# Kernel tuning notes

Hardware: AMD Instinct MI355X
Metric: run time of the kernel (lower is better)

## Reference

```python
import math
import jax, jax.numpy as jnp
import numpy as np

D_MODEL = 1024
D_K = 64
D_V = 64
N_HEADS = 16
D_HIDDEN = 4096
EPS = 1e-5


def setup_inputs() -> dict:
    key = jax.random.key(0)
    ks = jax.random.split(key, 10)
    s = 0.02
    x = jax.random.normal(ks[0], (2, 2048, D_MODEL), dtype=jnp.float32)
    wq = jax.random.normal(ks[1], (D_MODEL, D_K * N_HEADS), jnp.float32) * s
    bq = jnp.zeros((D_K * N_HEADS,), jnp.float32)
    wk = jax.random.normal(ks[2], (D_MODEL, D_K * N_HEADS), jnp.float32) * s
    bk = jnp.zeros((D_K * N_HEADS,), jnp.float32)
    wv = jax.random.normal(ks[3], (D_MODEL, D_V * N_HEADS), jnp.float32) * s
    bv = jnp.zeros((D_V * N_HEADS,), jnp.float32)
    wo = jax.random.normal(ks[4], (D_V * N_HEADS, D_MODEL), jnp.float32) * s
    ln1_g = jnp.ones((D_MODEL,), jnp.float32)
    ln1_b = jnp.zeros((D_MODEL,), jnp.float32)
    w1 = jax.random.normal(ks[5], (D_MODEL, D_HIDDEN), jnp.float32) * s
    b1 = jnp.zeros((D_HIDDEN,), jnp.float32)
    w2 = jax.random.normal(ks[6], (D_HIDDEN, D_MODEL), jnp.float32) * s
    ln2_g = jnp.ones((D_MODEL,), jnp.float32)
    ln2_b = jnp.zeros((D_MODEL,), jnp.float32)
    return dict(x=x, wq=wq, bq=bq, wk=wk, bk=bk, wv=wv, bv=bv, wo=wo,
                ln1_g=ln1_g, ln1_b=ln1_b, w1=w1, b1=b1, w2=w2,
                ln2_g=ln2_g, ln2_b=ln2_b)


def _layernorm(x, g, b):
    mu = jnp.mean(x, axis=-1, keepdims=True)
    var = jnp.mean((x - mu) ** 2, axis=-1, keepdims=True)
    return (x - mu) * jax.lax.rsqrt(var + EPS) * g + b


def reference(x, wq, bq, wk, bk, wv, bv, wo, ln1_g, ln1_b, w1, b1, w2, ln2_g, ln2_b):
    B, S, _ = x.shape
    split = lambda t, d: t.reshape(B, S, N_HEADS, d).transpose(0, 2, 1, 3)  # [B,H,S,d]
    Q = split(x @ wq + bq, D_K)
    K = split(x @ wk + bk, D_K)
    V = split(x @ wv + bv, D_V)
    scores = jnp.einsum('bhqd,bhkd->bhqk', Q / math.sqrt(D_K), K)
    causal = jnp.tril(jnp.ones((S, S), dtype=bool))
    scores = jnp.where(causal, scores, -jnp.inf)
    attn = jax.nn.softmax(scores, axis=-1)
    ctx = jnp.einsum('bhqk,bhkd->bhqd', attn, V)  # [B,H,S,d_v]
    merged = ctx.transpose(0, 2, 1, 3).reshape(B, S, N_HEADS * D_V)
    x = x + _layernorm(merged @ wo, ln1_g, ln1_b)
    h = jax.nn.gelu(x @ w1 + b1, approximate=False)
    x = x + _layernorm(h @ w2, ln2_g, ln2_b)
    return x
```

## Files before the change

### kernel.cpp

```cpp
#include <hip/hip_runtime.h>
#include <math.h>

typedef __bf16 bf16;
typedef __bf16 bf16x4 __attribute__((ext_vector_type(4)));
typedef __bf16 bf16x8 __attribute__((ext_vector_type(8)));
typedef float f32x4 __attribute__((ext_vector_type(4)));

#define MFMA16(a, b, c) __builtin_amdgcn_mfma_f32_16x16x32_bf16(a, b, c, 0, 0, 0)
#define QSCALE 0.180336879f
#define SSTR 3072
#define SOFT_M -14.0f

typedef __attribute__((address_space(3))) unsigned int lds_uint;
typedef const __attribute__((address_space(1))) unsigned int glb_uint;
__device__ __forceinline__ void gload_lds16(const void* g, void* l) {
    __builtin_amdgcn_global_load_lds((glb_uint*)g, (lds_uint*)l, 16, 0, 0);
}
__device__ __forceinline__ unsigned lds_addr(const void* p) {
    return (unsigned)(unsigned long long)(lds_uint*)p;
}

__global__ __launch_bounds__(256) void prep_kernel(
    const float* __restrict__ x,
    const float* __restrict__ wq, const float* __restrict__ wk,
    const float* __restrict__ wv, const float* __restrict__ wo,
    const float* __restrict__ w1, const float* __restrict__ w2,
    const float* __restrict__ bq, const float* __restrict__ bk,
    const float* __restrict__ bv,
    bf16* __restrict__ xbf, bf16* __restrict__ wqkvt, bf16* __restrict__ wot,
    bf16* __restrict__ w1t, bf16* __restrict__ w2t, float* __restrict__ bqkv) {
    const int bid = blockIdx.x, tid = threadIdx.x;
    if (bid < 4096) {
        size_t i = ((size_t)bid * 256 + tid) * 4;
        float4 v = *(const float4*)(x + i);
        bf16x4 o = {(bf16)v.x, (bf16)v.y, (bf16)v.z, (bf16)v.w};
        *(bf16x4*)(xbf + i) = o;
        return;
    }
    if (bid < 16384) {
        __shared__ float tile[32][33];
        const float* W; bf16* Wt; int K, N, n0, k0;
        if (bid < 8192) {
            int l = bid - 4096, z = l >> 10, t = l & 1023;
            W = z == 0 ? wq : z == 1 ? wk : z == 2 ? wv : wo;
            Wt = z == 3 ? wot : wqkvt + (size_t)z * 1024 * 1024;
            K = 1024; N = 1024; n0 = (t & 31) * 32; k0 = (t >> 5) * 32;
        } else if (bid < 12288) {
            int l = bid - 8192;
            W = w1; Wt = w1t; K = 1024; N = 4096;
            n0 = (l & 127) * 32; k0 = (l >> 7) * 32;
        } else {
            int l = bid - 12288;
            W = w2; Wt = w2t; K = 4096; N = 1024;
            n0 = (l & 31) * 32; k0 = (l >> 5) * 32;
        }
        const int tx = tid & 31, ty = tid >> 5;
        for (int i = 0; i < 32; i += 8)
            tile[ty + i][tx] = W[(size_t)(k0 + ty + i) * N + n0 + tx];
        __syncthreads();
        for (int i = 0; i < 32; i += 8)
            Wt[(size_t)(n0 + ty + i) * K + k0 + tx] = (bf16)tile[tx][ty + i];
        return;
    }
    int i = (bid - 16384) * 256 + tid;
    bqkv[i] = i < 1024 ? bq[i] : i < 2048 ? bk[i - 1024] : bv[i - 2048];
}

__global__ void transpose_v_kernel(const bf16* __restrict__ QKV, bf16* __restrict__ Vtg) {
    __shared__ bf16 t[64 * 64];
    const int tid = threadIdx.x;
    const int st = blockIdx.x;
    const int bh = blockIdx.y;
    const int b = bh >> 4, h = bh & 15;
    const bf16* src = QKV + (size_t)b * 2048 * SSTR + 2048 + h * 64 + (size_t)st * 64 * SSTR;
    const int s = tid >> 3, oct = tid & 7;
    bf16x8 v0 = *(const bf16x8*)&src[(size_t)s * SSTR + oct * 8];
    bf16x8 v1 = *(const bf16x8*)&src[(size_t)(s + 32) * SSTR + oct * 8];
    *(bf16x8*)&t[s * 64 + ((oct ^ (s & 7)) * 8)] = v0;
    *(bf16x8*)&t[(s + 32) * 64 + ((oct ^ (s & 7)) * 8)] = v1;
    __syncthreads();
    const int dv = tid >> 3, so = tid & 7;
    bf16 b0[8], b1[8];
#pragma unroll
    for (int j = 0; j < 8; j++) {
        int ss = (so & 4) * 8 + (so & 3) * 4 + (j < 4 ? j : 12 + j);
        b0[j] = t[ss * 64 + (((dv >> 3) ^ (ss & 7)) * 8) + (dv & 7)];
        b1[j] = t[ss * 64 + ((((dv + 32) >> 3) ^ (ss & 7)) * 8) + (dv & 7)];
    }
    bf16* dst = Vtg + (size_t)bh * 64 * 2048 + (size_t)st * 64;
    *(bf16x8*)&dst[(size_t)dv * 2048 + so * 8] = *(bf16x8*)b0;
    *(bf16x8*)&dst[(size_t)(dv + 32) * 2048 + so * 8] = *(bf16x8*)b1;
}

template <bool HAS_BIAS, bool DO_GELU, bool OUT_BF16, bool QKV_SCALE, int NSPLIT>
__global__ __launch_bounds__(256, 4) void gemm_nt(
    const bf16* __restrict__ A, const bf16* __restrict__ Bt,
    const float* __restrict__ bias,
    float* __restrict__ Cf, bf16* __restrict__ Cb,
    int M, int N, int K) {
    __shared__ bf16 As[2][128 * 32];
    __shared__ bf16 Bs[2][128 * 32];
    const int tid = threadIdx.x;
    const int wave = tid >> 6, lane = tid & 63;
    const int ln = lane & 15, quad = lane >> 4;
    const int GN = N >> 7;
    const int nblk = gridDim.x;
    const int bid = blockIdx.x;
    const int lid = (bid & 7) * (nblk >> 3) + (bid >> 3);
    const int ngroup = GN * 8;
    const int g = lid / ngroup, rem = lid - g * ngroup;
    const int m0 = (g * 8 + (rem & 7)) * 128;
    const int n0 = (rem >> 3) * 128;
    const int wm = (wave >> 1) * 64, wn = (wave & 1) * 64;
    int kz0 = 0, kz1 = K;
    if (NSPLIT > 1) {
        const int kchunk = K / NSPLIT;
        kz0 = blockIdx.z * kchunk;
        kz1 = kz0 + kchunk;
        if (OUT_BF16) Cb += (size_t)blockIdx.z * M * N;
        else          Cf += (size_t)blockIdx.z * M * N;
    }
    const int srow0 = wave * 32 + (lane >> 2);
    const int srow1 = srow0 + 16;
    const int soct = ((lane & 3) ^ (srow0 & 3)) * 8;
    const bf16* ga0 = A + (size_t)(m0 + srow0) * K + soct;
    const bf16* ga1 = A + (size_t)(m0 + srow1) * K + soct;
    const bf16* gb0 = Bt + (size_t)(n0 + srow0) * K + soct;
    const bf16* gb1 = Bt + (size_t)(n0 + srow1) * K + soct;

    f32x4 acc[4][4] = {};
    const int roct = (quad ^ (ln & 3)) * 8;

#define GSTAGE(k0_, bi_)                                        \
    {                                                           \
        bf16* la = As[bi_] + wave * 1024;                       \
        bf16* lb = Bs[bi_] + wave * 1024;                       \
        gload_lds16(ga0 + (k0_), la);                           \
        gload_lds16(ga1 + (k0_), la + 512);                     \
        gload_lds16(gb0 + (k0_), lb);                           \
        gload_lds16(gb1 + (k0_), lb + 512);                     \
    }

    GSTAGE(kz0, 0)
    int it = 0;
    for (int k0 = kz0; k0 < kz1; k0 += 32, ++it) {
        const int cur = it & 1;
        __syncthreads();
        if (k0 + 32 < kz1) GSTAGE(k0 + 32, cur ^ 1)
        bf16x8 af[4], bg[4];
#pragma unroll
        for (int i = 0; i < 4; i++) {
            af[i] = *(const bf16x8*)&As[cur][(wm + i * 16 + ln) * 32 + roct];
            bg[i] = *(const bf16x8*)&Bs[cur][(wn + i * 16 + ln) * 32 + roct];
        }
#pragma unroll
        for (int i = 0; i < 4; i++)
#pragma unroll
            for (int j = 0; j < 4; j++)
                acc[i][j] = MFMA16(af[i], bg[j], acc[i][j]);
    }
#undef GSTAGE

#pragma unroll
    for (int i = 0; i < 4; i++)
#pragma unroll
        for (int j = 0; j < 4; j++) {
            int col = n0 + wn + j * 16 + ln;
            float bv = HAS_BIAS ? bias[col] : 0.0f;
#pragma unroll
            for (int r = 0; r < 4; r++) {
                int row = m0 + wm + i * 16 + quad * 4 + r;
                float v = acc[i][j][r] + bv;
                if (QKV_SCALE && col < 1024) v *= QSCALE;
                if (DO_GELU) {
                    float u = v * (v * v * 0.044715f + 1.0f) * 0.7978845608f;
                    float t = __builtin_amdgcn_exp2f(u * 2.885390082f);
                    v = v * t * __builtin_amdgcn_rcpf(t + 1.0f);
                }
                if (OUT_BF16)
                    Cb[(size_t)row * N + col] = (bf16)v;
                else
                    Cf[(size_t)row * N + col] = v;
            }
        }
}

#define BARR() __builtin_amdgcn_s_barrier()
#define WAITLG(n_) { asm volatile("s_waitcnt lgkmcnt(" #n_ ")" ::: "memory"); \
                     __builtin_amdgcn_sched_barrier(0); }
#define WAITVM(n_) asm volatile("s_waitcnt vmcnt(" #n_ ")" ::: "memory")
#define PRIO1() __builtin_amdgcn_s_setprio(1)
#define PRIO0() __builtin_amdgcn_s_setprio(0)
#define DSR(d_, a_, o_) asm volatile("ds_read_b128 %0, %1 offset:%2" \
                                     : "=v"(d_) : "v"(a_), "i"(o_))

#define MF8K(KS_, IO_, NO_, BQ_) { \
    acc[(IO_) + 0][NO_]       = MFMA16(aF[0][KS_], BQ_[0][KS_], acc[(IO_) + 0][NO_]); \
    acc[(IO_) + 0][(NO_) + 1] = MFMA16(aF[0][KS_], BQ_[1][KS_], acc[(IO_) + 0][(NO_) + 1]); \
    acc[(IO_) + 1][NO_]       = MFMA16(aF[1][KS_], BQ_[0][KS_], acc[(IO_) + 1][NO_]); \
    acc[(IO_) + 1][(NO_) + 1] = MFMA16(aF[1][KS_], BQ_[1][KS_], acc[(IO_) + 1][(NO_) + 1]); \
    acc[(IO_) + 2][NO_]       = MFMA16(aF[2][KS_], BQ_[0][KS_], acc[(IO_) + 2][NO_]); \
    acc[(IO_) + 2][(NO_) + 1] = MFMA16(aF[2][KS_], BQ_[1][KS_], acc[(IO_) + 2][(NO_) + 1]); \
    acc[(IO_) + 3][NO_]       = MFMA16(aF[3][KS_], BQ_[0][KS_], acc[(IO_) + 3][NO_]); \
    acc[(IO_) + 3][(NO_) + 1] = MFMA16(aF[3][KS_], BQ_[1][KS_], acc[(IO_) + 3][(NO_) + 1]); }
#define MF16(IO_, NO_, BQ_) { MF8K(0, IO_, NO_, BQ_) MF8K(1, IO_, NO_, BQ_) }

template <bool HAS_BIAS, bool DO_GELU, bool QKV_SCALE, int NSPLIT>
__global__ __launch_bounds__(512, 2) void gemm256(
    const bf16* __restrict__ A, const bf16* __restrict__ Bt,
    const float* __restrict__ bias, bf16* __restrict__ Cb,
    int M, int N, int K) {
    __shared__ bf16 sh[65536];
    const int tid = threadIdx.x;
    const int wave = tid >> 6, lane = tid & 63;
    const int ln = lane & 15, quad = lane >> 4;
    const int wm = (wave >> 2) * 128, wn = (wave & 3) * 64;
    const int GN = N >> 8;
    const int nblk = gridDim.x;
    const int bid = blockIdx.x;
    const int lid = (bid & 7) * (nblk >> 3) + (bid >> 3);
    const int ngroup = GN * 8;
    const int gg = lid / ngroup, rem = lid - gg * ngroup;
    const int m0 = (gg * 8 + (rem & 7)) * 256;
    const int n0 = (rem >> 3) * 256;
    int kz0 = 0, KS = K;
    if (NSPLIT > 1) {
        KS = K / NSPLIT;
        kz0 = blockIdx.z * KS;
        Cb += (size_t)blockIdx.z * M * N;
    }
    const int NT = KS >> 6;

    const int lr = lane >> 3, lc = lane & 7;
    const int co = (lc ^ lr) * 8;
    const int hg0 = wave * 16 + lr, hg1 = hg0 + 8;
    const int rA0g0 = hg0 + (hg0 >= 64 ? 64 : 0);
    const int rA0g1 = hg1 + (hg1 >= 64 ? 64 : 0);
    const int rB0g0 = (hg0 >> 5) * 64 + (hg0 & 31);
    const int rB0g1 = (hg1 >> 5) * 64 + (hg1 & 31);
    const bf16* gA0 = A + (size_t)(m0 + rA0g0) * K + kz0 + co;
    const bf16* gA1 = A + (size_t)(m0 + rA0g1) * K + kz0 + co;
    const bf16* gB0 = Bt + (size_t)(n0 + rB0g0) * K + kz0 + co;
    const bf16* gB1 = Bt + (size_t)(n0 + rB0g1) * K + kz0 + co;
    const size_t aoff64 = (size_t)64 * K;
    const size_t boff32 = (size_t)32 * K;
    const int hA0 = wave * 16, hA1 = wave * 16 + 8;
    const int R0A0 = hA0 + (hA0 >= 64 ? 64 : 0);
    const int R0A1 = hA1 + (hA1 >= 64 ? 64 : 0);
    const int R0B0 = (hA0 >> 5) * 64 + (hA0 & 31);
    const int R0B1 = (hA1 >> 5) * 64 + (hA1 & 31);

#define ST_A0(B_, T_) do { \
    gload_lds16(gA0 + (size_t)(T_) * 64, sh + (B_) * 16384 + R0A0 * 64); \
    gload_lds16(gA1 + (size_t)(T_) * 64, sh + (B_) * 16384 + R0A1 * 64); } while (0)
#define ST_A1(B_, T_) do { \
    gload_lds16(gA0 + aoff64 + (size_t)(T_) * 64, sh + (B_) * 16384 + 4096 + R0A0 * 64); \
    gload_lds16(gA1 + aoff64 + (size_t)(T_) * 64, sh + (B_) * 16384 + 4096 + R0A1 * 64); } while (0)
#define ST_B0(B_, T_) do { \
    gload_lds16(gB0 + (size_t)(T_) * 64, sh + 32768 + (B_) * 16384 + R0B0 * 64); \
    gload_lds16(gB1 + (size_t)(T_) * 64, sh + 32768 + (B_) * 16384 + R0B1 * 64); } while (0)
#define ST_B1(B_, T_) do { \
    gload_lds16(gB0 + boff32 + (size_t)(T_) * 64, sh + 32768 + (B_) * 16384 + 2048 + R0B0 * 64); \
    gload_lds16(gB1 + boff32 + (size_t)(T_) * 64, sh + 32768 + (B_) * 16384 + 2048 + R0B1 * 64); } while (0)

    const unsigned lb = lds_addr(sh);
    unsigned aAdr[2][2], bAdr[2][2];
#pragma unroll
    for (int bu = 0; bu < 2; bu++)
#pragma unroll
        for (int ks = 0; ks < 2; ks++) {
            unsigned sw = (unsigned)(((ks * 4 + quad) ^ (ln & 7)) * 16);
            aAdr[bu][ks] = lb + bu * 32768u + (unsigned)(wm + ln) * 128u + sw;
            bAdr[bu][ks] = lb + 65536u + bu * 32768u + (unsigned)(wn + ln) * 128u + sw;
        }

    f32x4 acc[8][4] = {};
    bf16x8 aF[4][2], bQ0[2][2], bQ1[2][2];

#define RD_Q1(B_) { \
    DSR(aF[0][0], aAdr[B_][0], 0);     DSR(aF[0][1], aAdr[B_][1], 0); \
    DSR(aF[1][0], aAdr[B_][0], 2048);  DSR(aF[1][1], aAdr[B_][1], 2048); \
    DSR(aF[2][0], aAdr[B_][0], 4096);  DSR(aF[2][1], aAdr[B_][1], 4096); \
    DSR(aF[3][0], aAdr[B_][0], 6144);  DSR(aF[3][1], aAdr[B_][1], 6144); \
    DSR(bQ0[0][0], bAdr[B_][0], 0);    DSR(bQ0[0][1], bAdr[B_][1], 0); \
    DSR(bQ0[1][0], bAdr[B_][0], 2048); DSR(bQ0[1][1], bAdr[B_][1], 2048); }
#define RD_Q2(B_) { \
    DSR(bQ1[0][0], bAdr[B_][0], 4096); DSR(bQ1[0][1], bAdr[B_][1], 4096); \
    DSR(bQ1[1][0], bAdr[B_][0], 6144); DSR(bQ1[1][1], bAdr[B_][1], 6144); }
#define RD_Q3(B_) { \
    DSR(aF[0][0], aAdr[B_][0], 8192);  DSR(aF[1][0], aAdr[B_][0], 10240); \
    DSR(aF[2][0], aAdr[B_][0], 12288); DSR(aF[3][0], aAdr[B_][0], 14336); \
    DSR(aF[0][1], aAdr[B_][1], 8192);  DSR(aF[1][1], aAdr[B_][1], 10240); \
    DSR(aF[2][1], aAdr[B_][1], 12288); DSR(aF[3][1], aAdr[B_][1], 14336); }

    ST_A0(0, 0); ST_B0(0, 0);
    ST_B1(0, 0);
    ST_A1(0, 0);
    ST_A0(1, 1); ST_B0(1, 1);
    ST_B1(1, 1);
    WAITVM(6);
    BARR();
    RD_Q1(0);

#define TILE(B_, U_) { \
     \
    RD_Q2(B_); \
    WAITLG(4); PRIO1(); \
    MF16(0, 0, bQ0) \
    PRIO0(); \
    BARR();   \
     \
    if ((U_) + 2 < NT) { ST_A0(B_, (U_) + 2); ST_B0(B_, (U_) + 2); } \
    if ((U_) + 1 < NT) ST_A1((B_) ^ 1, (U_) + 1); \
     \
    WAITLG(0); PRIO1(); \
    MF16(0, 2, bQ1) \
    PRIO0(); \
     \
    if ((U_) < NT - 2) { WAITVM(6); } else { WAITVM(0); } \
    BARR();   \
     \
    if ((U_) + 2 < NT) ST_B1(B_, (U_) + 2); \
     \
    RD_Q3(B_); \
    WAITLG(4); PRIO1(); MF8K(0, 4, 0, bQ0) PRIO0(); \
    WAITLG(0); PRIO1(); MF8K(1, 4, 0, bQ0) PRIO0(); \
     \
    if ((U_) < NT - 2) { WAITVM(8); } else { WAITVM(0); } \
    BARR();   \
     \
    PRIO1(); \
    MF16(4, 2, bQ1) \
    PRIO0(); \
    if ((U_) + 1 < NT) RD_Q1((B_) ^ 1); \
}

    for (int u = 0; u < NT; u += 2) {
        TILE(0, u)
        TILE(1, u + 1)
    }
#undef TILE
#undef RD_Q1
#undef RD_Q2
#undef RD_Q3
#undef ST_A0
#undef ST_A1
#undef ST_B0
#undef ST_B1

#pragma unroll
    for (int i = 0; i < 8; i++)
#pragma unroll
        for (int j = 0; j < 4; j++) {
            int col = n0 + wn + j * 16 + ln;
            float bvv = HAS_BIAS ? bias[col] : 0.0f;
#pragma unroll
            for (int rr = 0; rr < 4; rr++) {
                int row = m0 + wm + i * 16 + quad * 4 + rr;
                float v = acc[i][j][rr] + bvv;
                if (QKV_SCALE && col < 1024) v *= QSCALE;
                if (DO_GELU) {
                    float u = v * (v * v * 0.044715f + 1.0f) * 0.7978845608f;
                    float t = __builtin_amdgcn_exp2f(u * 2.885390082f);
                    v = v * t * __builtin_amdgcn_rcpf(t + 1.0f);
                }
                Cb[(size_t)row * N + col] = (bf16)v;
            }
        }
}

__global__ __launch_bounds__(256, 4) void attn_kernel(
    const bf16* __restrict__ QKV, const bf16* __restrict__ Vtg,
    bf16* __restrict__ ctx) {
    __shared__ bf16 Ks[2][64 * 64];
    __shared__ bf16 Vs[2][64 * 64];
    const int tid = threadIdx.x, wave = tid >> 6, lane = tid & 63;
    const int ln = lane & 15, quad = lane >> 4;
    const int idx = blockIdx.x;
    const int qt = 31 - (idx >> 5);
    const int bh = idx & 31;
    const int b = bh >> 4, h = bh & 15;
    const size_t qkvbase = (size_t)b * 2048 * SSTR;
    const bf16* Qp = QKV + qkvbase + h * 64;
    const bf16* Kp = QKV + qkvbase + 1024 + h * 64;
    const bf16* Vtp = Vtg + (size_t)bh * 64 * 2048;
    const int qw = qt * 64 + wave * 16;
    const int qg = qw + ln;

    bf16x8 bq0 = *(const bf16x8*)&Qp[(size_t)qg * SSTR + quad * 8];
    bf16x8 bq1 = *(const bf16x8*)&Qp[(size_t)qg * SSTR + 32 + quad * 8];

    f32x4 o[4] = {};
    float l_run = 0.0f;

    const int kr = wave * 16 + (lane >> 3);
    const int koct = ((lane & 7) ^ (kr & 7)) * 8;
    const bf16* gk0 = Kp + (size_t)kr * SSTR + koct;
    const bf16* gk1 = Kp + (size_t)(kr + 8) * SSTR + koct;
    const bf16* gv0 = Vtp + (size_t)kr * 2048 + koct;
    const bf16* gv1 = Vtp + (size_t)(kr + 8) * 2048 + koct;

    const int nkt = qt + 1;
#define STAGE(kt_, bi_)                                                     \
    {                                                                       \
        const int kk = (kt_) * 64;                                          \
        bf16* lk = Ks[bi_] + wave * 1024;                                   \
        bf16* lv = Vs[bi_] + wave * 1024;                                   \
        gload_lds16(gk0 + (size_t)kk * SSTR, lk);                           \
        gload_lds16(gk1 + (size_t)kk * SSTR, lk + 512);                     \
        gload_lds16(gv0 + kk, lv);                                          \
        gload_lds16(gv1 + kk, lv + 512);                                    \
    }

    STAGE(0, 0)
    for (int kt = 0; kt < nkt; kt++) {
        const int cur = kt & 1;
        const int k0 = kt * 64;
        __syncthreads();
        if (kt + 1 < nkt) STAGE(kt + 1, cur ^ 1)

        const bf16* Kc = Ks[cur];
        const bf16* Vc = Vs[cur];
        f32x4 sc[4];
#pragma unroll
        for (int mt = 0; mt < 4; mt++) {
            sc[mt][0] = SOFT_M; sc[mt][1] = SOFT_M;
            sc[mt][2] = SOFT_M; sc[mt][3] = SOFT_M;
        }
        __builtin_amdgcn_s_setprio(1);
#pragma unroll
        for (int mt = 0; mt < 4; mt++) {
            const int sk = mt * 16 + ln, s7 = sk & 7;
            bf16x8 ka0 = *(const bf16x8*)&Kc[sk * 64 + ((quad ^ s7) * 8)];
            bf16x8 ka1 = *(const bf16x8*)&Kc[sk * 64 + (((quad + 4) ^ s7) * 8)];
            sc[mt] = MFMA16(ka0, bq0, sc[mt]);
            sc[mt] = MFMA16(ka1, bq1, sc[mt]);
        }
        __builtin_amdgcn_s_setprio(0);
        if (kt == qt) {
#pragma unroll
            for (int mt = 0; mt < 4; mt++)
#pragma unroll
                for (int r = 0; r < 4; r++) {
                    const int kg = k0 + mt * 16 + quad * 4 + r;
                    if (kg > qg) sc[mt][r] = -__builtin_inff();
                }
        }
        float sum = 0.0f;
#pragma unroll
        for (int mt = 0; mt < 4; mt++)
#pragma unroll
            for (int r = 0; r < 4; r++) {
                float pv = __builtin_amdgcn_exp2f(sc[mt][r]);
                sc[mt][r] = pv;
                sum += pv;
            }
        l_run += sum;

        bf16x8 pb0, pb1;
#pragma unroll
        for (int r = 0; r < 4; r++) {
            pb0[r]     = (bf16)sc[0][r];
            pb0[r + 4] = (bf16)sc[1][r];
            pb1[r]     = (bf16)sc[2][r];
            pb1[r + 4] = (bf16)sc[3][r];
        }
        __builtin_amdgcn_s_setprio(1);
#pragma unroll
        for (int nt = 0; nt < 4; nt++) {
            const int row = nt * 16 + ln, r7 = row & 7;
            bf16x8 va0 = *(const bf16x8*)&Vc[row * 64 + ((quad ^ r7) * 8)];
            bf16x8 va1 = *(const bf16x8*)&Vc[row * 64 + (((quad + 4) ^ r7) * 8)];
            o[nt] = MFMA16(va0, pb0, o[nt]);
            o[nt] = MFMA16(va1, pb1, o[nt]);
        }
        __builtin_amdgcn_s_setprio(0);
    }
#undef STAGE

    __syncthreads();
    l_run += __shfl_xor(l_run, 16);
    l_run += __shfl_xor(l_run, 32);
    const float inv = 1.0f / l_run;

    bf16* Ob = Ks[0] + wave * 1024;
#pragma unroll
    for (int nt = 0; nt < 4; nt++)
#pragma unroll
        for (int r = 0; r < 4; r++) {
            const int dvh = 2 * nt + (quad >> 1);
            const int dlo = (quad & 1) * 4 + r;
            Ob[ln * 64 + ((dvh ^ (ln & 7)) * 8) + dlo] = (bf16)(o[nt][r] * inv);
        }
    bf16* ctxp = ctx + (size_t)b * 2048 * 1024 + h * 64;
#pragma unroll
    for (int p2 = 0; p2 < 2; p2++) {
        const int qL = (lane >> 3) + 8 * p2;
        const int oct = lane & 7;
        bf16x8 v = *(const bf16x8*)&Ob[qL * 64 + ((oct ^ (qL & 7)) * 8)];
        *(bf16x8*)&ctxp[(size_t)(qw + qL) * 1024 + oct * 8] = v;
    }
}

template <int NPART>
__global__ __launch_bounds__(256) void ln_res_kernel(
    const float* res, const bf16* __restrict__ yb,
    const float* __restrict__ g, const float* __restrict__ beta,
    float* outf, bf16* __restrict__ outb) {
    const int row = blockIdx.x;
    const int tid = threadIdx.x;
    const size_t off = (size_t)row * 1024 + tid * 4;
    const size_t pstride = (size_t)4096 * 1024;
    float4 v = {0.0f, 0.0f, 0.0f, 0.0f};
#pragma unroll
    for (int pi = 0; pi < NPART; pi++) {
        bf16x4 a = *(const bf16x4*)(yb + pi * pstride + off);
        v.x += (float)a[0]; v.y += (float)a[1];
        v.z += (float)a[2]; v.w += (float)a[3];
    }
    float s = v.x + v.y + v.z + v.w;
    float s2 = v.x * v.x + v.y * v.y + v.z * v.z + v.w * v.w;
#pragma unroll
    for (int o = 1; o < 64; o <<= 1) {
        s += __shfl_xor(s, o);
        s2 += __shfl_xor(s2, o);
    }
    __shared__ float ws[8];
    const int wave = tid >> 6, lane = tid & 63;
    if (lane == 0) { ws[wave] = s; ws[4 + wave] = s2; }
    __syncthreads();
    s = ws[0] + ws[1] + ws[2] + ws[3];
    s2 = ws[4] + ws[5] + ws[6] + ws[7];
    float mu = s * (1.0f / 1024.0f);
    float var = s2 * (1.0f / 1024.0f) - mu * mu;
    float rs = rsqrtf(var + 1e-5f);
    float4 gv = *(const float4*)(g + tid * 4);
    float4 bv = *(const float4*)(beta + tid * 4);
    float4 rv = *(const float4*)(res + off);
    float4 ov;
    ov.x = rv.x + (v.x - mu) * rs * gv.x + bv.x;
    ov.y = rv.y + (v.y - mu) * rs * gv.y + bv.y;
    ov.z = rv.z + (v.z - mu) * rs * gv.z + bv.z;
    ov.w = rv.w + (v.w - mu) * rs * gv.w + bv.w;
    *(float4*)(outf + off) = ov;
    if (outb) {
        bf16x4 ob = {(bf16)ov.x, (bf16)ov.y, (bf16)ov.z, (bf16)ov.w};
        *(bf16x4*)(outb + off) = ob;
    }
}


extern "C" void kernel_launch(void* const* d_in, const int* in_sizes, int n_in,
                              void* d_out, int out_size, void* d_ws, size_t ws_size,
                              hipStream_t stream) {
    const float* x  = (const float*)d_in[0];
    const float* wq = (const float*)d_in[1];
    const float* bq = (const float*)d_in[2];
    const float* wk = (const float*)d_in[3];
    const float* bk = (const float*)d_in[4];
    const float* wv = (const float*)d_in[5];
    const float* bv = (const float*)d_in[6];
    const float* wo = (const float*)d_in[7];
    const float* g1 = (const float*)d_in[8];
    const float* be1 = (const float*)d_in[9];
    const float* w1 = (const float*)d_in[10];
    const float* b1 = (const float*)d_in[11];
    const float* w2 = (const float*)d_in[12];
    const float* g2 = (const float*)d_in[13];
    const float* be2 = (const float*)d_in[14];
    float* out = (float*)d_out;

    const int T = 4096;
    char* p = (char*)d_ws;
    auto take = [&](size_t n) { char* r = p; p += n; return r; };
    bf16* xbf   = (bf16*)take((size_t)T * 1024 * 2);
    bf16* wqkvt = (bf16*)take((size_t)3072 * 1024 * 2);
    float* bqkv = (float*)take(3072 * 4 + 4096);
    bf16* wot   = (bf16*)take(1024 * 1024 * 2);
    bf16* w1t   = (bf16*)take((size_t)4096 * 1024 * 2);
    bf16* w2t   = (bf16*)take((size_t)1024 * 4096 * 2);
    bf16* QKV   = (bf16*)take((size_t)T * 3072 * 2);
    bf16* ctx   = (bf16*)take((size_t)T * 1024 * 2);
    bf16* ypart = (bf16*)take((size_t)2 * T * 1024 * 2);
    bf16* Vtg   = (bf16*)take((size_t)32 * 64 * 2048 * 2);
    take((size_t)T * 1024 * 2);
    bf16* h   = QKV;
    bf16* x1b = xbf;
    float* x1 = out;

    prep_kernel<<<16396, 256, 0, stream>>>(x, wq, wk, wv, wo, w1, w2, bq, bk, bv,
                                           xbf, wqkvt, wot, w1t, w2t, bqkv);

    gemm_nt<true, false, true, true, 1><<<768, 256, 0, stream>>>(
        xbf, wqkvt, bqkv, nullptr, QKV, T, 3072, 1024);

    transpose_v_kernel<<<dim3(32, 32), 256, 0, stream>>>(QKV, Vtg);
    attn_kernel<<<1024, 256, 0, stream>>>(QKV, Vtg, ctx);

    gemm_nt<false, false, true, false, 2><<<dim3(256, 1, 2), 256, 0, stream>>>(
        ctx, wot, nullptr, nullptr, ypart, T, 1024, 1024);

    ln_res_kernel<2><<<T, 256, 0, stream>>>(x, ypart, g1, be1, x1, x1b);

    gemm256<true, true, false, 1><<<256, 512, 0, stream>>>(
        x1b, w1t, b1, h, T, 4096, 1024);

    gemm256<false, false, false, 4><<<dim3(64, 1, 4), 512, 0, stream>>>(
        h, w2t, nullptr, ypart, T, 1024, 4096);

    ln_res_kernel<4><<<T, 256, 0, stream>>>(x1, ypart, g2, be2, out, nullptr);
}
```

Before: 304.4 us.

## Load K and V tiles directly from global memory in attention, dropping LDS staging

The attention kernel no longer double-buffers K and V tiles in shared memory through async global-to-LDS loads with block barriers. Each wave now reads its K and V operands straight from global memory (relying on cache) and keeps only a small LDS buffer for the output transpose. This removes the per-tile barriers and LDS traffic and raises potential occupancy, but each of the four waves now fetches the same K/V data separately and loses the prefetch overlap.

```diff
diff --git a/kernel.cpp b/kernel.cpp
--- a/kernel.cpp
+++ b/kernel.cpp
@@ -372,8 +372,7 @@
 __global__ __launch_bounds__(256, 4) void attn_kernel(
     const bf16* __restrict__ QKV, const bf16* __restrict__ Vtg,
     bf16* __restrict__ ctx) {
-    __shared__ bf16 Ks[2][64 * 64];
-    __shared__ bf16 Vs[2][64 * 64];
+    __shared__ bf16 Ob_s[64 * 64];
     const int tid = threadIdx.x, wave = tid >> 6, lane = tid & 63;
     const int ln = lane & 15, quad = lane >> 4;
     const int idx = blockIdx.x;
@@ -393,50 +392,26 @@
     f32x4 o[4] = {};
     float l_run = 0.0f;
 
-    const int kr = wave * 16 + (lane >> 3);
-    const int koct = ((lane & 7) ^ (kr & 7)) * 8;
-    const bf16* gk0 = Kp + (size_t)kr * SSTR + koct;
-    const bf16* gk1 = Kp + (size_t)(kr + 8) * SSTR + koct;
-    const bf16* gv0 = Vtp + (size_t)kr * 2048 + koct;
-    const bf16* gv1 = Vtp + (size_t)(kr + 8) * 2048 + koct;
+    const bf16* Krow = Kp + (size_t)ln * SSTR;
+    const bf16* Vrow = Vtp + (size_t)ln * 2048;
 
     const int nkt = qt + 1;
-#define STAGE(kt_, bi_)                                                     \
-    {                                                                       \
-        const int kk = (kt_) * 64;                                          \
-        bf16* lk = Ks[bi_] + wave * 1024;                                   \
-        bf16* lv = Vs[bi_] + wave * 1024;                                   \
-        gload_lds16(gk0 + (size_t)kk * SSTR, lk);                           \
-        gload_lds16(gk1 + (size_t)kk * SSTR, lk + 512);                     \
-        gload_lds16(gv0 + kk, lv);                                          \
-        gload_lds16(gv1 + kk, lv + 512);                                    \
-    }
-
-    STAGE(0, 0)
     for (int kt = 0; kt < nkt; kt++) {
-        const int cur = kt & 1;
         const int k0 = kt * 64;
-        __syncthreads();
-        if (kt + 1 < nkt) STAGE(kt + 1, cur ^ 1)
-
-        const bf16* Kc = Ks[cur];
-        const bf16* Vc = Vs[cur];
         f32x4 sc[4];
 #pragma unroll
         for (int mt = 0; mt < 4; mt++) {
             sc[mt][0] = SOFT_M; sc[mt][1] = SOFT_M;
             sc[mt][2] = SOFT_M; sc[mt][3] = SOFT_M;
         }
-        __builtin_amdgcn_s_setprio(1);
 #pragma unroll
         for (int mt = 0; mt < 4; mt++) {
-            const int sk = mt * 16 + ln, s7 = sk & 7;
-            bf16x8 ka0 = *(const bf16x8*)&Kc[sk * 64 + ((quad ^ s7) * 8)];
-            bf16x8 ka1 = *(const bf16x8*)&Kc[sk * 64 + (((quad + 4) ^ s7) * 8)];
+            const bf16* kr = Krow + (size_t)(k0 + mt * 16) * SSTR;
+            bf16x8 ka0 = *(const bf16x8*)&kr[quad * 8];
+            bf16x8 ka1 = *(const bf16x8*)&kr[32 + quad * 8];
             sc[mt] = MFMA16(ka0, bq0, sc[mt]);
             sc[mt] = MFMA16(ka1, bq1, sc[mt]);
         }
-        __builtin_amdgcn_s_setprio(0);
         if (kt == qt) {
 #pragma unroll
             for (int mt = 0; mt < 4; mt++)
@@ -465,25 +440,21 @@
             pb1[r]     = (bf16)sc[2][r];
             pb1[r + 4] = (bf16)sc[3][r];
         }
-        __builtin_amdgcn_s_setprio(1);
 #pragma unroll
         for (int nt = 0; nt < 4; nt++) {
-            const int row = nt * 16 + ln, r7 = row & 7;
-            bf16x8 va0 = *(const bf16x8*)&Vc[row * 64 + ((quad ^ r7) * 8)];
-            bf16x8 va1 = *(const bf16x8*)&Vc[row * 64 + (((quad + 4) ^ r7) * 8)];
+            const bf16* vr = Vrow + (size_t)(nt * 16) * 2048 + k0;
+            bf16x8 va0 = *(const bf16x8*)&vr[quad * 8];
+            bf16x8 va1 = *(const bf16x8*)&vr[32 + quad * 8];
             o[nt] = MFMA16(va0, pb0, o[nt]);
             o[nt] = MFMA16(va1, pb1, o[nt]);
         }
-        __builtin_amdgcn_s_setprio(0);
-    }
-#undef STAGE
-
-    __syncthreads();
+    }
+
     l_run += __shfl_xor(l_run, 16);
     l_run += __shfl_xor(l_run, 32);
     const float inv = 1.0f / l_run;
 
-    bf16* Ob = Ks[0] + wave * 1024;
+    bf16* Ob = Ob_s + wave * 1024;
 #pragma unroll
     for (int nt = 0; nt < 4; nt++)
 #pragma unroll
```

After: 423.5 us. +39.1%, slower.
